# Kernel optimization log

Hardware: AMD Instinct MI355X
Metric: run time of the kernel (lower is better)

The kernel has to match this reference:

```python
import jax, jax.numpy as jnp
import numpy as np

B, T, D = 2, 2048, 2048
N, K, H = 16, 4, 128  # query heads, kv heads, head dim
G = N // K            # GQA groups
MIN_TS, MAX_TS = 1.0, 10000.0


def rope(x, positions):
    # x: [B, S, heads, H], positions: [B, S] int
    half = H // 2
    fraction = 2.0 * jnp.arange(half, dtype=jnp.float32) / H
    timescale = MIN_TS * (MAX_TS / MIN_TS) ** fraction            # [half]
    sinusoid = positions.astype(jnp.float32)[:, :, None, None] / timescale  # [B,S,1,half]
    sin, cos = jnp.sin(sinusoid), jnp.cos(sinusoid)
    x1, x2 = x[..., :half], x[..., half:]
    return jnp.concatenate([x1 * cos - x2 * sin, x2 * cos + x1 * sin], axis=-1)


def setup_inputs() -> dict:
    key = jax.random.key(0)
    ks = jax.random.split(key, 6)
    pos = jnp.tile(jnp.arange(T, dtype=jnp.int32)[None, :], (B, 1))
    return {
        "Xq": jax.random.normal(ks[0], (B, T, D), jnp.float32),
        "Xkv": jax.random.normal(ks[1], (B, T, D), jnp.float32),
        "q_positions": pos,
        "kv_positions": pos,
        "Wq": jax.random.normal(ks[2], (D, N, H), jnp.float32) * 0.02,
        "Wk": jax.random.normal(ks[3], (D, K, H), jnp.float32) * 0.02,
        "Wv": jax.random.normal(ks[4], (D, K, H), jnp.float32) * 0.02,
        "Wo": jax.random.normal(ks[5], (N, H, D), jnp.float32) * 0.02,
    }


def reference(Xq, Xkv, q_positions, kv_positions, Wq, Wk, Wv, Wo):
    # QKV projections (tensordot over embed dim), fp32
    q = jnp.einsum("btd,dnh->btnh", Xq, Wq)          # [B,T,N,H]
    k = jnp.einsum("bsd,dkh->bskh", Xkv, Wk)         # [B,S,K,H]
    v = jnp.einsum("bsd,dkh->bskh", Xkv, Wv)
    # inline RoPE on q and k
    q = rope(q, q_positions)
    k = rope(k, kv_positions)
    # GQA: group query heads over kv heads -> [B,K,G,T,H]
    qg = q.transpose(0, 2, 1, 3).reshape(B, K, G, T, H)
    kt = k.transpose(0, 2, 1, 3)                      # [B,K,S,H]
    vt = v.transpose(0, 2, 1, 3)
    scale = 1.0 / jnp.sqrt(jnp.float32(H))
    scores = jnp.einsum("bkgth,bksh->bkgts", qg, kt) * scale
    # causal mask (self-attn, no explicit mask, T>1)
    causal = jnp.tril(jnp.ones((T, T), dtype=bool))
    scores = jnp.where(causal[None, None, None], scores, jnp.finfo(scores.dtype).min)
    probs = jax.nn.softmax(scores, axis=-1)
    attn = jnp.einsum("bkgts,bksh->bkgth", probs, vt)  # [B,K,G,T,H]
    attn = attn.reshape(B, N, T, H).transpose(0, 2, 1, 3)  # [B,T,N,H]
    out = jnp.einsum("btnh,nhd->btd", attn, Wo)
    return out
```

## Files before the change

kernel.cpp:

```cpp
#include <hip/hip_runtime.h>
#include <hip/hip_bf16.h>
#include <cstdint>
#include <cstddef>

#define Bdim 2
#define Tdim 2048
#define Ddim 2048
#define NHq  16
#define NKV  4
#define HD   128
#define SCALE 0.08838834764831845f
#define QPRESCALE (0.08838834764831845f * 1.4426950408889634f)
#define NEG_INF (-3.0e38f)
#define DEFER_THR 11.5f

typedef unsigned short u16;
typedef unsigned int   u32;
typedef __bf16 bf16x8 __attribute__((ext_vector_type(8)));
typedef float  f32x4  __attribute__((ext_vector_type(4)));

__device__ __forceinline__ u16 f2bf(float f) {
    unsigned int u = __float_as_uint(f);
    u += 0x7FFFu + ((u >> 16) & 1u);
    return (u16)(u >> 16);
}
__device__ __forceinline__ u16 f2bfn(float f) {
    __bf16 h = (__bf16)f;
    return __builtin_bit_cast(u16, h);
}
__device__ __forceinline__ float bf2f(u16 s) {
    return __uint_as_float(((unsigned int)s) << 16);
}

#if __has_builtin(__builtin_amdgcn_permlane16_swap) && __has_builtin(__builtin_amdgcn_permlane32_swap)
#define HAVE_PERMLANE_SWAP 1
#endif

__device__ __forceinline__ float quad_reduce_max(float v) {
#ifdef HAVE_PERMLANE_SWAP
    auto r = __builtin_amdgcn_permlane16_swap(__float_as_uint(v), __float_as_uint(v), false, false);
    float m = fmaxf(__uint_as_float(r[0]), __uint_as_float(r[1]));
    auto r2 = __builtin_amdgcn_permlane32_swap(__float_as_uint(m), __float_as_uint(m), false, false);
    return fmaxf(__uint_as_float(r2[0]), __uint_as_float(r2[1]));
#else
    v = fmaxf(v, __shfl_xor(v, 16));
    return fmaxf(v, __shfl_xor(v, 32));
#endif
}
__device__ __forceinline__ float quad_reduce_sum(float v) {
#ifdef HAVE_PERMLANE_SWAP
    auto r = __builtin_amdgcn_permlane16_swap(__float_as_uint(v), __float_as_uint(v), false, false);
    float s = __uint_as_float(r[0]) + __uint_as_float(r[1]);
    auto r2 = __builtin_amdgcn_permlane32_swap(__float_as_uint(s), __float_as_uint(s), false, false);
    return __uint_as_float(r2[0]) + __uint_as_float(r2[1]);
#else
    v += __shfl_xor(v, 16);
    return v + __shfl_xor(v, 32);
#endif
}

__device__ __forceinline__ float tree_max16(const float (&s)[16]) {
    float a0 = fmaxf(s[0], s[1]),  a1 = fmaxf(s[2], s[3]);
    float a2 = fmaxf(s[4], s[5]),  a3 = fmaxf(s[6], s[7]);
    float a4 = fmaxf(s[8], s[9]),  a5 = fmaxf(s[10], s[11]);
    float a6 = fmaxf(s[12], s[13]), a7 = fmaxf(s[14], s[15]);
    float b0 = fmaxf(a0, a1), b1 = fmaxf(a2, a3);
    float b2 = fmaxf(a4, a5), b3 = fmaxf(a6, a7);
    return fmaxf(fmaxf(b0, b1), fmaxf(b2, b3));
}
__device__ __forceinline__ float tree_sum16(const float (&s)[16]) {
    float a0 = s[0] + s[1],  a1 = s[2] + s[3];
    float a2 = s[4] + s[5],  a3 = s[6] + s[7];
    float a4 = s[8] + s[9],  a5 = s[10] + s[11];
    float a6 = s[12] + s[13], a7 = s[14] + s[15];
    float b0 = a0 + a1, b1 = a2 + a3, b2 = a4 + a5, b3 = a6 + a7;
    return (b0 + b1) + (b2 + b3);
}

typedef __attribute__((address_space(1))) const u32 gbl_u32;
typedef __attribute__((address_space(3))) u32 lds_u32;
__device__ __forceinline__ void gload16(const void* g, void* l) {
    __builtin_amdgcn_global_load_lds((gbl_u32*)(uintptr_t)g, (lds_u32*)(uintptr_t)l, 16, 0, 0);
}

#define VM8 asm volatile("s_waitcnt vmcnt(8)" ::: "memory")
#define VM4 asm volatile("s_waitcnt vmcnt(4)" ::: "memory")
#define VM0 asm volatile("s_waitcnt vmcnt(0)" ::: "memory")
#define VMNONE ((void)0)
#define BARRIER do { asm volatile("" ::: "memory"); __builtin_amdgcn_s_barrier(); asm volatile("" ::: "memory"); } while (0)

__global__ __launch_bounds__(256) void cvt_x(const float* __restrict__ Xq,
                                             const float* __restrict__ Xkv,
                                             u16* __restrict__ oq,
                                             u16* __restrict__ okv)
{
    const size_t NE = (size_t)4096 * 2048 / 8;
    size_t idx = (size_t)blockIdx.x * 256 + threadIdx.x;
    const float* src; u16* dst; size_t off;
    if (idx < NE) { src = Xq;  dst = oq;  off = idx * 8; }
    else          { src = Xkv; dst = okv; off = (idx - NE) * 8; }
    float4 a = *(const float4*)&src[off];
    float4 b = *(const float4*)&src[off + 4];
    ushort4 r0, r1;
    r0.x = f2bf(a.x); r0.y = f2bf(a.y); r0.z = f2bf(a.z); r0.w = f2bf(a.w);
    r1.x = f2bf(b.x); r1.y = f2bf(b.y); r1.z = f2bf(b.z); r1.w = f2bf(b.w);
    *(ushort4*)&dst[off] = r0;
    *(ushort4*)&dst[off + 4] = r1;
}

__global__ __launch_bounds__(256) void cvt_w_t(const float* __restrict__ src,
                                               u16* __restrict__ dst, int R, int C)
{
    __shared__ u16 t[64][72];
    const int r0 = blockIdx.y * 64, c0 = blockIdx.x * 64;
    const int tid = threadIdx.x;
    const int tr = tid >> 4, tc4 = (tid & 15) * 4;
#pragma unroll
    for (int p = 0; p < 4; p++) {
        int r = p * 16 + tr;
        float4 v = *(const float4*)&src[(size_t)(r0 + r) * C + c0 + tc4];
        t[tc4 + 0][r] = f2bf(v.x);
        t[tc4 + 1][r] = f2bf(v.y);
        t[tc4 + 2][r] = f2bf(v.z);
        t[tc4 + 3][r] = f2bf(v.w);
    }
    __syncthreads();
#pragma unroll
    for (int p = 0; p < 4; p++) {
        int cc = p * 16 + tr;
        ushort4 w = *(const ushort4*)&t[cc][tc4];
        *(ushort4*)&dst[(size_t)(c0 + cc) * R + r0 + tc4] = w;
    }
}

#define GPH(c, ks, mh, STAGE, VMW) do {                                        \
    bf16x8 Af[4];                                                              \
    _Pragma("unroll")                                                          \
    for (int mf = 0; mf < 4; mf++)                                             \
        Af[mf] = *(const bf16x8*)&Ab[c][ks][(arow + (mh) * 64 + mf * 16) * 32 + cxs]; \
    if ((mh) == 0) {                                                           \
        _Pragma("unroll")                                                      \
        for (int nf = 0; nf < 4; nf++)                                         \
            Bf[nf] = *(const bf16x8*)&Bb[c][ks][(brow + nf * 16) * 32 + cxs];  \
    }                                                                          \
    STAGE;                                                                     \
    BARRIER;                                                                   \
    asm volatile("s_waitcnt lgkmcnt(0)" ::: "memory");                         \
    __builtin_amdgcn_s_setprio(1);                                             \
    _Pragma("unroll")                                                          \
    for (int mf = 0; mf < 4; mf++)                                             \
        _Pragma("unroll")                                                      \
        for (int nf = 0; nf < 4; nf++)                                         \
            acc[(mh) * 4 + mf][nf] = __builtin_amdgcn_mfma_f32_16x16x32_bf16(  \
                Af[mf], Bf[nf], acc[(mh) * 4 + mf][nf], 0, 0, 0);              \
    __builtin_amdgcn_s_setprio(0);                                             \
    VMW;                                                                       \
    BARRIER;                                                                   \
} while (0)

__device__ __forceinline__ void gemm8_mainloop(const u16* __restrict__ A,
                                               const u16* __restrict__ Bt,
                                               int m0, int n0,
                                               u16 (&Ab)[2][2][256 * 32],
                                               u16 (&Bb)[2][2][256 * 32],
                                               f32x4 (&acc)[8][4])
{
    const int tid = threadIdx.x;
    const int wv = tid >> 6, lane = tid & 63;
    const int l15 = lane & 15, quad = lane >> 4;
    const int wr = wv >> 2, wc = wv & 3;

#pragma unroll
    for (int mf = 0; mf < 8; mf++)
#pragma unroll
        for (int nf = 0; nf < 4; nf++) acc[mf][nf] = (f32x4){0.f, 0.f, 0.f, 0.f};

    auto stageA = [&](int kt, int kh, int c) {
#pragma unroll
        for (int j = 0; j < 2; j++) {
            int q = j * 512 + tid;
            int r = q >> 2;
            int c4 = (q & 3) ^ (r & 3);
            gload16(A + (size_t)(m0 + r) * 2048 + kt * 64 + kh * 32 + c4 * 8,
                    &Ab[c][kh][q * 8]);
        }
    };
    auto stageB = [&](int kt, int kh, int c) {
#pragma unroll
        for (int j = 0; j < 2; j++) {
            int q = j * 512 + tid;
            int r = q >> 2;
            int c4 = (q & 3) ^ (r & 3);
            gload16(Bt + (size_t)(n0 + r) * 2048 + kt * 64 + kh * 32 + c4 * 8,
                    &Bb[c][kh][q * 8]);
        }
    };

    const int arow = wr * 128 + l15;
    const int brow = wc * 64 + l15;
    const int cxs  = (quad ^ (l15 & 3)) * 8;

    stageA(0, 0, 0); stageB(0, 0, 0);
    stageA(0, 1, 0); stageB(0, 1, 0);
    stageA(1, 0, 1); stageB(1, 0, 1);
    VM8;
    BARRIER;

    bf16x8 Bf[4];
    for (int it = 0; it < 15; it++) {
        const int t0 = 2 * it, t1 = 2 * it + 1;
        GPH(0, 0, 0, { stageA(t1, 1, 1); },     VMNONE);
        GPH(0, 0, 1, { stageB(t1, 1, 1); },     VM8);
        GPH(0, 1, 0, { stageA(t0 + 2, 0, 0); }, VMNONE);
        GPH(0, 1, 1, { stageB(t0 + 2, 0, 0); }, VM8);
        GPH(1, 0, 0, { stageA(t0 + 2, 1, 0); }, VMNONE);
        GPH(1, 0, 1, { stageB(t0 + 2, 1, 0); }, VM8);
        GPH(1, 1, 0, { stageA(t1 + 2, 0, 1); }, VMNONE);
        GPH(1, 1, 1, { stageB(t1 + 2, 0, 1); }, VM8);
    }
    GPH(0, 0, 0, { stageA(31, 1, 1); }, VMNONE);
    GPH(0, 0, 1, { stageB(31, 1, 1); }, VM8);
    GPH(0, 1, 0, VMNONE, VMNONE);
    GPH(0, 1, 1, VMNONE, VM4);
    GPH(1, 0, 0, VMNONE, VMNONE);
    GPH(1, 0, 1, VMNONE, VM0);
    GPH(1, 1, 0, VMNONE, VMNONE);
    GPH(1, 1, 1, VMNONE, VMNONE);
}

__global__ __launch_bounds__(512, 2) void qkv_gemm8(const u16* __restrict__ Xq,
                                                    const u16* __restrict__ Xkv,
                                                    const u16* __restrict__ Wqt,
                                                    const u16* __restrict__ Wkt,
                                                    const u16* __restrict__ Wvt,
                                                    u16* __restrict__ qraw,
                                                    u16* __restrict__ kraw,
                                                    u16* __restrict__ vt)
{
    __shared__ __align__(16) u16 Ab[2][2][256 * 32];
    __shared__ __align__(16) u16 Bb[2][2][256 * 32];
    f32x4 acc[8][4];

    const int bid0 = (int)blockIdx.x + 12 * (int)blockIdx.y;
    const int swz  = (bid0 & 7) * 24 + (bid0 >> 3);
    const int cx   = swz % 12;
    const int m0   = (swz / 12) * 256;

    const u16 *A, *Bt; int nb;
    if (cx < 8)       { A = Xq;  Bt = Wqt; nb = cx * 256; }
    else if (cx < 10) { A = Xkv; Bt = Wkt; nb = (cx - 8) * 256; }
    else              { A = Xkv; Bt = Wvt; nb = (cx - 10) * 256; }

    gemm8_mainloop(A, Bt, m0, nb, Ab, Bb, acc);

    const int tid = threadIdx.x;
    const int wv = tid >> 6, lane = tid & 63;
    const int l15 = lane & 15, quad = lane >> 4;
    const int wr = wv >> 2, wc = wv & 3;
    const int row0 = m0 + wr * 128;

    if (cx < 10) {
        u16* out; int ldw;
        if (cx < 8) { out = qraw; ldw = 2048; }
        else        { out = kraw; ldw = 512; }
#pragma unroll
        for (int mf = 0; mf < 8; mf++)
#pragma unroll
            for (int nf = 0; nf < 4; nf++) {
                int col = nb + wc * 64 + nf * 16 + l15;
                int r = row0 + mf * 16 + quad * 4;
#pragma unroll
                for (int reg = 0; reg < 4; reg++)
                    out[(size_t)(r + reg) * ldw + col] = f2bf(acc[mf][nf][reg]);
            }
    } else {
        const int b = m0 >> 11;
#pragma unroll
        for (int mf = 0; mf < 8; mf++)
#pragma unroll
            for (int nf = 0; nf < 4; nf++) {
                int col = nb + wc * 64 + nf * 16 + l15;
                int tloc = ((row0 & 2047) + mf * 16 + quad * 4);
                ushort4 w4;
                w4.x = f2bf(acc[mf][nf][0]);
                w4.y = f2bf(acc[mf][nf][1]);
                w4.z = f2bf(acc[mf][nf][2]);
                w4.w = f2bf(acc[mf][nf][3]);
                *(ushort4*)&vt[((size_t)(b * 512 + col)) * 2048 + tloc] = w4;
            }
    }
}

__global__ __launch_bounds__(512, 2) void oproj_gemm8(const u16* __restrict__ attnb,
                                                      const u16* __restrict__ Wot,
                                                      float* __restrict__ out)
{
    __shared__ __align__(16) u16 Ab[2][2][256 * 32];
    __shared__ __align__(16) u16 Bb[2][2][256 * 32];
    f32x4 acc[8][4];

    const int bid0 = (int)blockIdx.x + 8 * (int)blockIdx.y;
    const int swz  = (bid0 & 7) * 16 + (bid0 >> 3);
    const int n0   = (swz % 8) * 256;
    const int m0   = (swz / 8) * 256;

    gemm8_mainloop(attnb, Wot, m0, n0, Ab, Bb, acc);

    const int tid = threadIdx.x;
    const int wv = tid >> 6, lane = tid & 63;
    const int l15 = lane & 15, quad = lane >> 4;
    const int wr = wv >> 2, wc = wv & 3;
    const int row0 = m0 + wr * 128;
#pragma unroll
    for (int mf = 0; mf < 8; mf++)
#pragma unroll
        for (int nf = 0; nf < 4; nf++) {
            int col = n0 + wc * 64 + nf * 16 + l15;
            int r = row0 + mf * 16 + quad * 4;
#pragma unroll
            for (int reg = 0; reg < 4; reg++)
                out[(size_t)(r + reg) * 2048 + col] = acc[mf][nf][reg];
        }
}

__global__ __launch_bounds__(256) void rope_bf(u16* __restrict__ q,
                                               u16* __restrict__ k,
                                               const int* __restrict__ qpos,
                                               const int* __restrict__ kvpos)
{
    const int qTh = Bdim * Tdim * NHq * 16;
    int idx = blockIdx.x * 256 + threadIdx.x;
    u16* base; int h4; int pos; float osc;
    if (idx < qTh) {
        int rn = idx >> 4; h4 = (idx & 15) * 4;
        pos = qpos[rn >> 4];
        base = q + (size_t)rn * HD;
        osc = QPRESCALE;
    } else {
        int j = idx - qTh;
        int rn = j >> 4; h4 = (j & 15) * 4;
        pos = kvpos[rn >> 2];
        base = k + (size_t)rn * HD;
        osc = 1.0f;
    }
    ushort4 a = *(const ushort4*)&base[h4];
    ushort4 bvec = *(const ushort4*)&base[h4 + 64];
    u16 av[4] = {a.x, a.y, a.z, a.w};
    u16 bv[4] = {bvec.x, bvec.y, bvec.z, bvec.w};
#pragma unroll
    for (int j = 0; j < 4; j++) {
        float inv_ts = expf(-(float)(h4 + j) * 0.14391156831f);
        float ang = (float)pos * inv_ts;
        float s, c;
        sincosf(ang, &s, &c);
        s *= osc; c *= osc;
        float x1 = bf2f(av[j]), x2 = bf2f(bv[j]);
        av[j] = f2bf(x1 * c - x2 * s);
        bv[j] = f2bf(x2 * c + x1 * s);
    }
    ushort4 ra, rb;
    ra.x = av[0]; ra.y = av[1]; ra.z = av[2]; ra.w = av[3];
    rb.x = bv[0]; rb.y = bv[1]; rb.z = bv[2]; rb.w = bv[3];
    *(ushort4*)&base[h4] = ra;
    *(ushort4*)&base[h4 + 64] = rb;
}

__global__ __launch_bounds__(512, 4) void flash_attn_v5(const u16* __restrict__ qh,
                                                        const u16* __restrict__ kh,
                                                        const u16* __restrict__ vtg,
                                                        u16* __restrict__ attnb)
{
    __shared__ __align__(16) u16 Ks[2][64 * 128];
    __shared__ __align__(16) u16 Vt[2][128 * 64];
    __shared__ __align__(16) u16 Ps[128 * 64];

    const int yy = blockIdx.y;
    const int qt = (yy < 8) ? (15 - yy) : (yy - 8);
    const int bh = blockIdx.x;
    const int b = bh >> 4, n = bh & 15, kvh = n >> 2;
    const int q0 = qt * 128;
    const int tid = threadIdx.x;
    const int wv = tid >> 6, lane = tid & 63;
    const int l15 = lane & 15, quad = lane >> 4;

    const size_t kbase = (size_t)(b * Tdim) * 512 + kvh * 128;
    const size_t vbase = ((size_t)(b * 512 + kvh * 128)) * 2048;
    const int nT = 2 * qt + 2;

    auto stage = [&](int t, int buf) {
        const int s0s = t * 64;
#pragma unroll
        for (int c = 0; c < 2; c++) {
            int j = c * 512 + tid;
            int s = j >> 4;
            int c8 = (j & 15) ^ (s & 7);
            gload16(kh + kbase + (size_t)(s0s + s) * 512 + c8 * 8,
                    &Ks[buf][(c * 512 + wv * 64) * 8]);
            int h = j >> 3;
            int sb = (j & 7) ^ (h & 7);
            gload16(vtg + vbase + (size_t)h * 2048 + s0s + sb * 8,
                    &Vt[buf][(c * 512 + wv * 64) * 8]);
        }
    };

    stage(0, 0);

    bf16x8 qfrag[4];
    {
        const size_t qbase = ((size_t)(b * Tdim + q0 + wv * 16)) * 2048 + n * 128;
#pragma unroll
        for (int kt = 0; kt < 4; kt++)
            qfrag[kt] = *(const bf16x8*)(qh + qbase + (size_t)l15 * 2048
                                          + kt * 32 + quad * 8);
    }

    f32x4 Oacc[8];
#pragma unroll
    for (int ht = 0; ht < 8; ht++) Oacc[ht] = (f32x4){0.f, 0.f, 0.f, 0.f};
    float mrow = NEG_INF;
    float lrow = 0.f;

    __syncthreads();

    int cur = 0;
    for (int t = 0; t < nT; t++) {
        const int s0 = t * 64;

        if (t + 1 < nT) stage(t + 1, cur ^ 1);

        f32x4 S[4];
#pragma unroll
        for (int nt = 0; nt < 4; nt++) S[nt] = (f32x4){0.f, 0.f, 0.f, 0.f};
#pragma unroll
        for (int kt = 0; kt < 4; kt++) {
            bf16x8 kf[4];
#pragma unroll
            for (int nt = 0; nt < 4; nt++) {
                int s = nt * 16 + l15;
                int cb = (kt * 4 + quad) ^ (s & 7);
                kf[nt] = *(const bf16x8*)&Ks[cur][s * 128 + cb * 8];
            }
#pragma unroll
            for (int nt = 0; nt < 4; nt++)
                S[nt] = __builtin_amdgcn_mfma_f32_16x16x32_bf16(kf[nt], qfrag[kt], S[nt], 0, 0, 0);
        }

        const bool domask = (t >= nT - 2);
        const int m_l = wv * 16 + l15;
        const int mg = q0 + m_l;
        float sv[16];
#pragma unroll
        for (int nt = 0; nt < 4; nt++)
#pragma unroll
            for (int r = 0; r < 4; r++) {
                float vv = S[nt][r];
                if (domask) {
                    int sg = s0 + nt * 16 + quad * 4 + r;
                    if (sg > mg) vv = NEG_INF;
                }
                sv[nt * 4 + r] = vv;
            }
        float mx = quad_reduce_max(tree_max16(sv));
        const bool skip = __all(mx <= mrow + DEFER_THR);
        const float mNew = skip ? mrow : fmaxf(mrow, mx);
#pragma unroll
        for (int i = 0; i < 16; i++)
            sv[i] = __builtin_amdgcn_exp2f(sv[i] - mNew);
#pragma unroll
        for (int nt = 0; nt < 4; nt++) {
            int sb = nt * 2 + (quad >> 1);
            int cb = sb ^ (m_l & 7);
            ushort4 pw;
            pw.x = f2bfn(sv[nt * 4 + 0]);
            pw.y = f2bfn(sv[nt * 4 + 1]);
            pw.z = f2bfn(sv[nt * 4 + 2]);
            pw.w = f2bfn(sv[nt * 4 + 3]);
            *(ushort4*)&Ps[m_l * 64 + cb * 8 + (quad & 1) * 4] = pw;
        }
        {
            float ps = quad_reduce_sum(tree_sum16(sv));
            if (skip) {
                lrow += ps;
            } else {
                float alpha = __builtin_amdgcn_exp2f(mrow - mNew);
                mrow = mNew;
                lrow = lrow * alpha + ps;
                float a0 = __shfl(alpha, quad * 4 + 0);
                float a1 = __shfl(alpha, quad * 4 + 1);
                float a2 = __shfl(alpha, quad * 4 + 2);
                float a3 = __shfl(alpha, quad * 4 + 3);
#pragma unroll
                for (int ht = 0; ht < 8; ht++) {
                    Oacc[ht][0] *= a0;
                    Oacc[ht][1] *= a1;
                    Oacc[ht][2] *= a2;
                    Oacc[ht][3] *= a3;
                }
            }
        }

#pragma unroll
        for (int k2 = 0; k2 < 2; k2++) {
            int cbp = (k2 * 4 + quad) ^ (m_l & 7);
            bf16x8 pf = *(const bf16x8*)&Ps[m_l * 64 + cbp * 8];
#pragma unroll
            for (int ht = 0; ht < 8; ht++) {
                int h = ht * 16 + l15;
                int cb = (k2 * 4 + quad) ^ (h & 7);
                bf16x8 vf = *(const bf16x8*)&Vt[cur][h * 64 + cb * 8];
                Oacc[ht] = __builtin_amdgcn_mfma_f32_16x16x32_bf16(pf, vf, Oacc[ht], 0, 0, 0);
            }
        }

        __syncthreads();
        cur ^= 1;
    }

    {
        f32x4 inv;
#pragma unroll
        for (int r = 0; r < 4; r++)
            inv[r] = 1.0f / __shfl(lrow, quad * 4 + r);
        int mg0 = q0 + wv * 16 + quad * 4;
        u16* dst0 = attnb + ((size_t)(b * Tdim + mg0)) * 2048 + n * 128 + l15;
#pragma unroll
        for (int ht = 0; ht < 8; ht++) {
#pragma unroll
            for (int r = 0; r < 4; r++)
                dst0[(size_t)r * 2048 + ht * 16] = f2bfn(Oacc[ht][r] * inv[r]);
        }
    }
}

extern "C" void kernel_launch(void* const* d_in, const int* in_sizes, int n_in,
                              void* d_out, int out_size, void* d_ws, size_t ws_size,
                              hipStream_t stream) {
    const float* Xq    = (const float*)d_in[0];
    const float* Xkv   = (const float*)d_in[1];
    const int*   qpos  = (const int*)d_in[2];
    const int*   kvpos = (const int*)d_in[3];
    const float* Wq    = (const float*)d_in[4];
    const float* Wk    = (const float*)d_in[5];
    const float* Wv    = (const float*)d_in[6];
    const float* Wo    = (const float*)d_in[7];
    float* out = (float*)d_out;

    char* w = (char*)d_ws;
    u16* xq_bf = (u16*)(w);
    u16* xkv_bf= (u16*)(w + (16u << 20));
    u16* qraw  = (u16*)(w + (32u << 20));
    u16* kraw  = (u16*)(w + (48u << 20));
    u16* vt    = (u16*)(w + (52u << 20));
    u16* wq_t  = (u16*)(w + (56u << 20));
    u16* wk_t  = (u16*)(w + (64u << 20));
    u16* wv_t  = (u16*)(w + (66u << 20));
    u16* wo_t  = (u16*)(w + (68u << 20));
    u16* attnb = (u16*)(w);

    cvt_x<<<8192, 256, 0, stream>>>(Xq, Xkv, xq_bf, xkv_bf);
    cvt_w_t<<<dim3(32, 32), 256, 0, stream>>>(Wq, wq_t, 2048, 2048);
    cvt_w_t<<<dim3(8, 32),  256, 0, stream>>>(Wk, wk_t, 2048, 512);
    cvt_w_t<<<dim3(8, 32),  256, 0, stream>>>(Wv, wv_t, 2048, 512);
    cvt_w_t<<<dim3(32, 32), 256, 0, stream>>>(Wo, wo_t, 2048, 2048);
    qkv_gemm8<<<dim3(12, 16), 512, 0, stream>>>(xq_bf, xkv_bf, wq_t, wk_t, wv_t,
                                                qraw, kraw, vt);
    rope_bf<<<5120, 256, 0, stream>>>(qraw, kraw, qpos, kvpos);
    flash_attn_v5<<<dim3(32, 16), 512, 0, stream>>>(qraw, kraw, vt, attnb);
    oproj_gemm8<<<dim3(8, 16), 512, 0, stream>>>(attnb, wo_t, out);
}
```

Before: 349.1 us.

## Fuse RoPE into QKV GEMM and attention, merge prep kernels into one launch

Removes the standalone rope_bf kernel. K RoPE is applied in the QKV GEMM epilogue, using a permutation of the Wk columns so that each lane holds both rotation halves. Q RoPE and the softmax prescale are applied while loading Q fragments in the attention kernel. The four conversion/transpose kernels are merged into a single prep_all launch. This drops one full read-modify-write pass over q/k and several launch overheads, but adds sincos work to the GEMM epilogue and attention prologue.

```diff
diff --git a/kernel.cpp b/kernel.cpp
--- a/kernel.cpp
+++ b/kernel.cpp
@@ -89,31 +89,47 @@
 #define VMNONE ((void)0)
 #define BARRIER do { asm volatile("" ::: "memory"); __builtin_amdgcn_s_barrier(); asm volatile("" ::: "memory"); } while (0)
 
-__global__ __launch_bounds__(256) void cvt_x(const float* __restrict__ Xq,
-                                             const float* __restrict__ Xkv,
-                                             u16* __restrict__ oq,
-                                             u16* __restrict__ okv)
-{
-    const size_t NE = (size_t)4096 * 2048 / 8;
-    size_t idx = (size_t)blockIdx.x * 256 + threadIdx.x;
-    const float* src; u16* dst; size_t off;
-    if (idx < NE) { src = Xq;  dst = oq;  off = idx * 8; }
-    else          { src = Xkv; dst = okv; off = (idx - NE) * 8; }
-    float4 a = *(const float4*)&src[off];
-    float4 b = *(const float4*)&src[off + 4];
-    ushort4 r0, r1;
-    r0.x = f2bf(a.x); r0.y = f2bf(a.y); r0.z = f2bf(a.z); r0.w = f2bf(a.w);
-    r1.x = f2bf(b.x); r1.y = f2bf(b.y); r1.z = f2bf(b.z); r1.w = f2bf(b.w);
-    *(ushort4*)&dst[off] = r0;
-    *(ushort4*)&dst[off + 4] = r1;
-}
-
-__global__ __launch_bounds__(256) void cvt_w_t(const float* __restrict__ src,
-                                               u16* __restrict__ dst, int R, int C)
+__global__ __launch_bounds__(256) void prep_all(const float* __restrict__ Xq,
+                                                const float* __restrict__ Xkv,
+                                                const float* __restrict__ Wq,
+                                                const float* __restrict__ Wk,
+                                                const float* __restrict__ Wv,
+                                                const float* __restrict__ Wo,
+                                                u16* __restrict__ xq_bf,
+                                                u16* __restrict__ xkv_bf,
+                                                u16* __restrict__ wq_t,
+                                                u16* __restrict__ wk_t,
+                                                u16* __restrict__ wv_t,
+                                                u16* __restrict__ wo_t)
 {
     __shared__ u16 t[64][72];
-    const int r0 = blockIdx.y * 64, c0 = blockIdx.x * 64;
     const int tid = threadIdx.x;
+    int bid = blockIdx.x;
+
+    if (bid < 8192) {
+        const size_t NE = (size_t)4096 * 2048 / 8;
+        size_t idx = (size_t)bid * 256 + tid;
+        const float* src; u16* dst; size_t off;
+        if (idx < NE) { src = Xq;  dst = xq_bf;  off = idx * 8; }
+        else          { src = Xkv; dst = xkv_bf; off = (idx - NE) * 8; }
+        float4 a = *(const float4*)&src[off];
+        float4 b = *(const float4*)&src[off + 4];
+        ushort4 r0, r1;
+        r0.x = f2bf(a.x); r0.y = f2bf(a.y); r0.z = f2bf(a.z); r0.w = f2bf(a.w);
+        r1.x = f2bf(b.x); r1.y = f2bf(b.y); r1.z = f2bf(b.z); r1.w = f2bf(b.w);
+        *(ushort4*)&dst[off] = r0;
+        *(ushort4*)&dst[off + 4] = r1;
+        return;
+    }
+    bid -= 8192;
+    const float* src; u16* dst; int C, gx; bool kperm = false;
+    const int R = 2048;
+    if (bid < 1024)      { src = Wq; dst = wq_t; C = 2048; gx = 32; }
+    else if (bid < 1280) { src = Wk; dst = wk_t; C = 512;  gx = 8;  bid -= 1024; kperm = true; }
+    else if (bid < 1536) { src = Wv; dst = wv_t; C = 512;  gx = 8;  bid -= 1280; }
+    else                 { src = Wo; dst = wo_t; C = 2048; gx = 32; bid -= 1536; }
+
+    const int r0 = (bid / gx) * 64, c0 = (bid % gx) * 64;
     const int tr = tid >> 4, tc4 = (tid & 15) * 4;
 #pragma unroll
     for (int p = 0; p < 4; p++) {
@@ -128,8 +144,14 @@
 #pragma unroll
     for (int p = 0; p < 4; p++) {
         int cc = p * 16 + tr;
+        int rr = c0 + cc;
+        if (kperm) {
+            int h = rr & 127;
+            rr = (rr & ~127) | (h & 15) | (((h >> 6) & 1) << 4)
+               | (((h >> 4) & 1) << 5) | (((h >> 5) & 1) << 6);
+        }
         ushort4 w = *(const ushort4*)&t[cc][tc4];
-        *(ushort4*)&dst[(size_t)(c0 + cc) * R + r0 + tc4] = w;
+        *(ushort4*)&dst[(size_t)rr * R + r0 + tc4] = w;
     }
 }
 
@@ -233,6 +255,7 @@
                                                     const u16* __restrict__ Wqt,
                                                     const u16* __restrict__ Wkt,
                                                     const u16* __restrict__ Wvt,
+                                                    const int* __restrict__ kvpos,
                                                     u16* __restrict__ qraw,
                                                     u16* __restrict__ kraw,
                                                     u16* __restrict__ vt)
@@ -259,10 +282,7 @@
     const int wr = wv >> 2, wc = wv & 3;
     const int row0 = m0 + wr * 128;
 
-    if (cx < 10) {
-        u16* out; int ldw;
-        if (cx < 8) { out = qraw; ldw = 2048; }
-        else        { out = kraw; ldw = 512; }
+    if (cx < 8) {
 #pragma unroll
         for (int mf = 0; mf < 8; mf++)
 #pragma unroll
@@ -271,8 +291,33 @@
                 int r = row0 + mf * 16 + quad * 4;
 #pragma unroll
                 for (int reg = 0; reg < 4; reg++)
-                    out[(size_t)(r + reg) * ldw + col] = f2bf(acc[mf][nf][reg]);
-            }
+                    qraw[(size_t)(r + reg) * 2048 + col] = f2bf(acc[mf][nf][reg]);
+            }
+    } else if (cx < 10) {
+        const int b = m0 >> 11;
+        const int t0r = (m0 & 2047) + wr * 128;
+        const int kvh = (nb >> 7) + (wc >> 1);
+        const int hb0 = ((wc & 1) << 5) | l15;
+#pragma unroll
+        for (int pair = 0; pair < 2; pair++) {
+            const int h = hb0 | (pair << 4);
+            const float inv_ts = expf(-(float)h * 0.14391156831f);
+#pragma unroll
+            for (int mf = 0; mf < 8; mf++) {
+#pragma unroll
+                for (int reg = 0; reg < 4; reg++) {
+                    int trr = t0r + mf * 16 + quad * 4 + reg;
+                    int pos = kvpos[b * 2048 + trr];
+                    float s, c;
+                    sincosf((float)pos * inv_ts, &s, &c);
+                    float x1 = acc[mf][pair * 2 + 0][reg];
+                    float x2 = acc[mf][pair * 2 + 1][reg];
+                    u16* kp = kraw + ((size_t)(b * 2048 + trr)) * 512 + kvh * 128 + h;
+                    kp[0]  = f2bf(x1 * c - x2 * s);
+                    kp[64] = f2bf(x2 * c + x1 * s);
+                }
+            }
+        }
     } else {
         const int b = m0 >> 11;
 #pragma unroll
@@ -323,51 +368,10 @@
         }
 }
 
-__global__ __launch_bounds__(256) void rope_bf(u16* __restrict__ q,
-                                               u16* __restrict__ k,
-                                               const int* __restrict__ qpos,
-                                               const int* __restrict__ kvpos)
-{
-    const int qTh = Bdim * Tdim * NHq * 16;
-    int idx = blockIdx.x * 256 + threadIdx.x;
-    u16* base; int h4; int pos; float osc;
-    if (idx < qTh) {
-        int rn = idx >> 4; h4 = (idx & 15) * 4;
-        pos = qpos[rn >> 4];
-        base = q + (size_t)rn * HD;
-        osc = QPRESCALE;
-    } else {
-        int j = idx - qTh;
-        int rn = j >> 4; h4 = (j & 15) * 4;
-        pos = kvpos[rn >> 2];
-        base = k + (size_t)rn * HD;
-        osc = 1.0f;
-    }
-    ushort4 a = *(const ushort4*)&base[h4];
-    ushort4 bvec = *(const ushort4*)&base[h4 + 64];
-    u16 av[4] = {a.x, a.y, a.z, a.w};
-    u16 bv[4] = {bvec.x, bvec.y, bvec.z, bvec.w};
-#pragma unroll
-    for (int j = 0; j < 4; j++) {
-        float inv_ts = expf(-(float)(h4 + j) * 0.14391156831f);
-        float ang = (float)pos * inv_ts;
-        float s, c;
-        sincosf(ang, &s, &c);
-        s *= osc; c *= osc;
-        float x1 = bf2f(av[j]), x2 = bf2f(bv[j]);
-        av[j] = f2bf(x1 * c - x2 * s);
-        bv[j] = f2bf(x2 * c + x1 * s);
-    }
-    ushort4 ra, rb;
-    ra.x = av[0]; ra.y = av[1]; ra.z = av[2]; ra.w = av[3];
-    rb.x = bv[0]; rb.y = bv[1]; rb.z = bv[2]; rb.w = bv[3];
-    *(ushort4*)&base[h4] = ra;
-    *(ushort4*)&base[h4 + 64] = rb;
-}
-
-__global__ __launch_bounds__(512, 4) void flash_attn_v5(const u16* __restrict__ qh,
+__global__ __launch_bounds__(512, 4) void flash_attn_v6(const u16* __restrict__ qh,
                                                         const u16* __restrict__ kh,
                                                         const u16* __restrict__ vtg,
+                                                        const int* __restrict__ qpos,
                                                         u16* __restrict__ attnb)
 {
     __shared__ __align__(16) u16 Ks[2][64 * 128];
@@ -408,10 +412,35 @@
     bf16x8 qfrag[4];
     {
         const size_t qbase = ((size_t)(b * Tdim + q0 + wv * 16)) * 2048 + n * 128;
-#pragma unroll
-        for (int kt = 0; kt < 4; kt++)
-            qfrag[kt] = *(const bf16x8*)(qh + qbase + (size_t)l15 * 2048
-                                          + kt * 32 + quad * 8);
+        float qv[4][8];
+#pragma unroll
+        for (int kt = 0; kt < 4; kt++) {
+            bf16x8 raw = *(const bf16x8*)(qh + qbase + (size_t)l15 * 2048
+                                           + kt * 32 + quad * 8);
+#pragma unroll
+            for (int j = 0; j < 8; j++) qv[kt][j] = (float)raw[j];
+        }
+        const int pos = qpos[b * Tdim + q0 + wv * 16 + l15];
+#pragma unroll
+        for (int kt = 0; kt < 2; kt++)
+#pragma unroll
+            for (int j = 0; j < 8; j++) {
+                int h = kt * 32 + quad * 8 + j;
+                float inv_ts = expf(-(float)h * 0.14391156831f);
+                float s, c;
+                sincosf((float)pos * inv_ts, &s, &c);
+                s *= QPRESCALE; c *= QPRESCALE;
+                float x1 = qv[kt][j], x2 = qv[kt + 2][j];
+                qv[kt][j]     = x1 * c - x2 * s;
+                qv[kt + 2][j] = x2 * c + x1 * s;
+            }
+#pragma unroll
+        for (int kt = 0; kt < 4; kt++) {
+            bf16x8 f;
+#pragma unroll
+            for (int j = 0; j < 8; j++) f[j] = (__bf16)qv[kt][j];
+            qfrag[kt] = f;
+        }
     }
 
     f32x4 Oacc[8];
@@ -557,14 +586,10 @@
     u16* wo_t  = (u16*)(w + (68u << 20));
     u16* attnb = (u16*)(w);
 
-    cvt_x<<<8192, 256, 0, stream>>>(Xq, Xkv, xq_bf, xkv_bf);
-    cvt_w_t<<<dim3(32, 32), 256, 0, stream>>>(Wq, wq_t, 2048, 2048);
-    cvt_w_t<<<dim3(8, 32),  256, 0, stream>>>(Wk, wk_t, 2048, 512);
-    cvt_w_t<<<dim3(8, 32),  256, 0, stream>>>(Wv, wv_t, 2048, 512);
-    cvt_w_t<<<dim3(32, 32), 256, 0, stream>>>(Wo, wo_t, 2048, 2048);
+    prep_all<<<10752, 256, 0, stream>>>(Xq, Xkv, Wq, Wk, Wv, Wo,
+                                        xq_bf, xkv_bf, wq_t, wk_t, wv_t, wo_t);
     qkv_gemm8<<<dim3(12, 16), 512, 0, stream>>>(xq_bf, xkv_bf, wq_t, wk_t, wv_t,
-                                                qraw, kraw, vt);
-    rope_bf<<<5120, 256, 0, stream>>>(qraw, kraw, qpos, kvpos);
-    flash_attn_v5<<<dim3(32, 16), 512, 0, stream>>>(qraw, kraw, vt, attnb);
+                                                kvpos, qraw, kraw, vt);
+    flash_attn_v6<<<dim3(32, 16), 512, 0, stream>>>(qraw, kraw, vt, qpos, attnb);
     oproj_gemm8<<<dim3(8, 16), 512, 0, stream>>>(attnb, wo_t, out);
 }
```

Result: slower. 374.7 us (+7.3%).
